# Kernel optimization log

Hardware: AMD Instinct MI355X
Metric: run time of the kernel (lower is better)

The kernel has to match this reference:

```python
import jax, jax.numpy as jnp
import numpy as np

# static sizes (see shape_source)
OBJ_N, WALL_N, FLOOR_N = 192, 16, 1
T = OBJ_N + WALL_N + FLOOR_N          # 209 total nodes
R = T * T - T                          # 43472 directed edges (no self loops)
D = 512
STEPS = 4                              # feat_update_step (1 group)
OBJ_IN, WALL_IN, FLOOR_IN, REL_IN = 42, 15, 16, 2

# buildMap: all-pairs meshgrid edges, self-loops removed, one-hot subj/obj maps
_nd = ~np.eye(T, dtype=bool)
_si, _oi = np.meshgrid(np.arange(T), np.arange(T), indexing='ij')
_subj_idx = _si[_nd]
_obj_idx = _oi[_nd]
SUBJ_MAP = jnp.asarray((np.arange(T)[:, None] == _subj_idx[None, :]).astype(np.float32))  # [T,R]
OBJ_MAP = jnp.asarray((np.arange(T)[:, None] == _obj_idx[None, :]).astype(np.float32))    # [T,R]
TOTAL_MAP = jnp.ones((T, T), jnp.float32)
REL_IDX = jnp.asarray(np.nonzero(_nd.reshape(-1))[0])  # [R] static gather indices


def setup_inputs():
    key = jax.random.key(0)
    ks = iter(jax.random.split(key, 64))
    def w(shape):
        return jax.random.normal(next(ks), shape, jnp.float32) * 0.01  # normal_(0, 0.01)
    inp = {
        'cat_object_feature': jax.random.normal(next(ks), (1, OBJ_N, OBJ_IN), jnp.float32),
        'cat_wall_feature': jax.random.normal(next(ks), (1, WALL_N, WALL_IN), jnp.float32),
        'cat_floor_feature': jax.random.normal(next(ks), (1, FLOOR_N, FLOOR_IN), jnp.float32),
        'cat_relation_feature': jax.random.normal(next(ks), (1, OBJ_N * OBJ_N, REL_IN), jnp.float32),
    }
    for name, din in [('obj', OBJ_IN), ('wall', WALL_IN), ('floor', FLOOR_IN), ('rel', REL_IN)]:
        inp[name + '_w1'] = w((din, D)); inp[name + '_b1'] = jnp.zeros((D,), jnp.float32)
        inp[name + '_w2'] = w((D, D));   inp[name + '_b2'] = jnp.zeros((D,), jnp.float32)
    inp['collect_w'] = w((5, D, D))                       # 5 _Collection_Unit fc weights
    inp['collect_b'] = jnp.zeros((5, D), jnp.float32)
    for name in ['tr', 'eu', 'sc']:
        inp[name + '_w1'] = w((D, D // 2)); inp[name + '_b1'] = jnp.zeros((D // 2,), jnp.float32)
        inp[name + '_w2'] = w((D // 2, 3)); inp[name + '_b2'] = jnp.zeros((3,), jnp.float32)
    return inp


def _mlp(x, w1, b1, w2, b2):
    return jax.nn.relu(x @ w1 + b1) @ w2 + b2


def _head(x, w1, b1, w2, b2):
    # Linear -> LeakyReLU(0.2) -> Dropout(eval: identity) -> Linear
    return jax.nn.leaky_relu(x @ w1 + b1, 0.2) @ w2 + b2


def _collect(src, attn, w, b):
    # _Collection_Unit: attn @ relu(fc(src)) / (row_sum + 1e-7)
    fc = jax.nn.relu(src @ w + b)
    return (attn @ fc) / (attn.sum(1, keepdims=True) + 1e-7)


def reference(cat_object_feature, cat_wall_feature, cat_floor_feature, cat_relation_feature,
              obj_w1, obj_b1, obj_w2, obj_b2, wall_w1, wall_b1, wall_w2, wall_b2,
              floor_w1, floor_b1, floor_w2, floor_b2, rel_w1, rel_b1, rel_w2, rel_b2,
              collect_w, collect_b, tr_w1, tr_b1, tr_w2, tr_b2,
              eu_w1, eu_b1, eu_w2, eu_b2, sc_w1, sc_b1, sc_w2, sc_b2):
    tot = jnp.concatenate([
        _mlp(cat_object_feature[0], obj_w1, obj_b1, obj_w2, obj_b2),
        _mlp(cat_wall_feature[0], wall_w1, wall_b1, wall_w2, wall_b2),
        _mlp(cat_floor_feature[0], floor_w1, floor_b1, floor_w2, floor_b2)], axis=0)  # [T,D]
    emb_rel = _mlp(cat_relation_feature[0], rel_w1, rel_b1, rel_w2, rel_b2)
    padded = jnp.pad(emb_rel.reshape(OBJ_N, OBJ_N, D),
                     ((0, T - OBJ_N), (0, T - OBJ_N), (0, 0)), constant_values=0.001)
    rel = padded.reshape(T * T, D)[REL_IDX]  # mask_total_relation_feature [R,D]

    for _ in range(STEPS):
        s_obj = _collect(tot, TOTAL_MAP, collect_w[4], collect_b[4])
        s_rs = _collect(rel, SUBJ_MAP, collect_w[0], collect_b[0])
        s_ro = _collect(rel, OBJ_MAP, collect_w[1], collect_b[1])
        new_tot = tot + (s_obj + s_rs + s_ro) / 3.0          # _Update_Unit: target + source
        s_os = _collect(tot, SUBJ_MAP.T, collect_w[2], collect_b[2])
        s_oo = _collect(tot, OBJ_MAP.T, collect_w[3], collect_b[3])
        rel = rel + (s_os + s_oo) / 2.0
        tot = new_tot

    obj = tot[:OBJ_N]  # object_mask select
    return jnp.concatenate([
        _head(obj, tr_w1, tr_b1, tr_w2, tr_b2),
        _head(obj, eu_w1, eu_b1, eu_w2, eu_b2),
        _head(obj, sc_w1, sc_b1, sc_w2, sc_b2)], axis=-1)  # [OBJ_N, 9]
```

## Files before the change

### kernel.cpp

```cpp
#include <hip/hip_runtime.h>
#include <stdint.h>

typedef unsigned short u16;
typedef __attribute__((ext_vector_type(4))) float f32x4;
typedef __attribute__((ext_vector_type(8))) short s16x8;
typedef __attribute__((ext_vector_type(4))) short s16x4;

#define DD (512*512)

__device__ inline u16 f2bf(float f) {
  uint32_t u = __float_as_uint(f);
  u = (u + 0x7FFFu + ((u >> 16) & 1u)) >> 16;
  return (u16)u;
}
__device__ inline float bflo(uint32_t w) { return __uint_as_float(w << 16); }
__device__ inline float bfhi(uint32_t w) { return __uint_as_float(w & 0xFFFF0000u); }
__device__ inline f32x4 relu4(f32x4 v) {
  f32x4 r;
  r.x = fmaxf(v.x, 0.f); r.y = fmaxf(v.y, 0.f);
  r.z = fmaxf(v.z, 0.f); r.w = fmaxf(v.w, 0.f);
  return r;
}
__device__ inline f32x4 bf4(const u16* p) {
  uint2 w = *(const uint2*)p;
  f32x4 r; r.x = bflo(w.x); r.y = bfhi(w.x); r.z = bflo(w.y); r.w = bfhi(w.y);
  return r;
}
__device__ inline s16x4 pack4(f32x4 v) {
  s16x4 o;
  o[0] = (short)f2bf(v.x); o[1] = (short)f2bf(v.y);
  o[2] = (short)f2bf(v.z); o[3] = (short)f2bf(v.w);
  return o;
}
__device__ inline void gload16(const void* g, void* l) {
  __builtin_amdgcn_global_load_lds(
      (const __attribute__((address_space(1))) void*)g,
      (__attribute__((address_space(3))) void*)l, 16, 0, 0);
}

struct PrepP {
  const float *xo, *xw, *xf;
  const float *ow1, *ob1, *ww1, *wb1, *fw1, *fb1;
  float* hid;
  const float* rw2; u16* rw2b;
  const float* cw; u16* cwT;
  const float* cb; const float* rb2;
  float *b0b, *b0p, *b1b, *b1p;
  const float *xr, *rw1, *rb1; u16* Hh;
};

__global__ __launch_bounds__(256) void kprep(PrepP pp) {
  __shared__ __align__(16) float plds[1088];
  const int bid = blockIdx.x;
  const int t = threadIdx.x;
  if (bid < 209) {
    int tc = bid;
    const float* x; const float* w; const float* b; int K;
    if (tc < 192)      { x = pp.xo + tc * 42;         w = pp.ow1; b = pp.ob1; K = 42; }
    else if (tc < 208) { x = pp.xw + (tc - 192) * 15; w = pp.ww1; b = pp.wb1; K = 15; }
    else               { x = pp.xf;                   w = pp.fw1; b = pp.fb1; K = 16; }
    float* xs = plds;
    if (t < K) xs[t] = x[t];
    __syncthreads();
    #pragma unroll
    for (int dd = 0; dd < 2; dd++) {
      int d = t + dd * 256;
      float acc = b[d];
      for (int k = 0; k < K; k++) acc = fmaf(xs[k], w[k * 512 + d], acc);
      pp.hid[(size_t)tc * 512 + d] = fmaxf(acc, 0.f);
    }
  } else if (bid < 337) {
    int g = (bid - 209) * 256 + t;
    f32x4 a = *(const f32x4*)&pp.rw2[(size_t)g * 8];
    f32x4 b = *(const f32x4*)&pp.rw2[(size_t)g * 8 + 4];
    s16x8 o;
    o[0] = (short)f2bf(a.x); o[1] = (short)f2bf(a.y); o[2] = (short)f2bf(a.z); o[3] = (short)f2bf(a.w);
    o[4] = (short)f2bf(b.x); o[5] = (short)f2bf(b.y); o[6] = (short)f2bf(b.z); o[7] = (short)f2bf(b.w);
    *(s16x8*)&pp.rw2b[(size_t)g * 8] = o;
  } else if (bid < 1617) {
    int local = bid - 337;
    int bx = local & 15, by = (local >> 4) & 15, bz = local >> 8;
    float (*tile)[33] = (float(*)[33])plds;
    const float* src = pp.cw + (size_t)bz * DD;
    int k0 = bx * 32, n0 = by * 32;
    #pragma unroll
    for (int i = 0; i < 4; i++) {
      int idx = t + i * 256; int r = idx >> 5, c = idx & 31;
      tile[r][c] = src[(size_t)(k0 + r) * 512 + n0 + c];
    }
    __syncthreads();
    #pragma unroll
    for (int i = 0; i < 4; i++) {
      int idx = t + i * 256; int r = idx >> 5, c = idx & 31;
      pp.cwT[((size_t)bz * 512 + n0 + r) * 512 + k0 + c] = f2bf(tile[c][r]);
    }
  } else if (bid < 1625) {
    int bx = bid - 1617;
    int dl = t & 63;
    int d = bx * 64 + dl;
    int kg = t >> 6;
    const float* W0 = pp.cw;
    const float* W1 = pp.cw + DD;
    float a0 = 0, p0 = 0, a1 = 0, p1 = 0;
    for (int k = kg * 128; k < (kg + 1) * 128; ++k) {
      float w0 = W0[(size_t)k * 512 + d], w1 = W1[(size_t)k * 512 + d], r = pp.rb2[k];
      a0 = fmaf(r, w0, a0); p0 += w0;
      a1 = fmaf(r, w1, a1); p1 += w1;
    }
    float (*red)[4][64] = (float(*)[4][64])plds;
    red[0][kg][dl] = a0; red[1][kg][dl] = p0; red[2][kg][dl] = a1; red[3][kg][dl] = p1;
    __syncthreads();
    if (kg == 0) {
      float s0  = red[0][0][dl] + red[0][1][dl] + red[0][2][dl] + red[0][3][dl];
      float sp0 = red[1][0][dl] + red[1][1][dl] + red[1][2][dl] + red[1][3][dl];
      float s1  = red[2][0][dl] + red[2][1][dl] + red[2][2][dl] + red[2][3][dl];
      float sp1 = red[3][0][dl] + red[3][1][dl] + red[3][2][dl] + red[3][3][dl];
      float bb0 = pp.cb[0 * 512 + d], bb1 = pp.cb[1 * 512 + d];
      pp.b0b[d] = s0 + bb0;
      pp.b0p[d] = 0.001f * sp0 + bb0;
      pp.b1b[d] = s1 + bb1;
      pp.b1p[d] = 0.001f * sp1 + bb1;
    }
  } else {
    int gid = (bid - 1625) * 256 + t;
    int m = gid >> 6;
    int dg = (gid & 63) * 8;
    float x0 = pp.xr[m * 2], x1 = pp.xr[m * 2 + 1];
    s16x8 o;
    #pragma unroll
    for (int j = 0; j < 8; j++) {
      int dd = dg + j;
      float v = fmaf(x0, pp.rw1[dd], fmaf(x1, pp.rw1[512 + dd], pp.rb1[dd]));
      o[j] = (short)f2bf(fmaxf(v, 0.f));
    }
    *(s16x8*)&pp.Hh[(size_t)m * 512 + dg] = o;
  }
}

struct SJob { const float* A; const float* B; const float* bias; float* C; u16* Cb; int M; int act; };
struct SJobs { SJob j[4]; int cum[5]; int njobs; };
struct PMJob { const u16* A; const u16* BT; u16* W; };
struct MidP { SJobs sj; PMJob mj[2]; };

__global__ __launch_bounds__(256) void kmid(MidP mp) {
  __shared__ __align__(16) u16 mlds[24576];
  const int t = threadIdx.x;
  if (blockIdx.x < 64) {
    int bi = blockIdx.x;
    int ji = 0;
    while (ji + 1 < mp.sj.njobs && bi >= mp.sj.cum[ji + 1]) ji++;
    SJob job = mp.sj.j[ji];
    int local = bi - mp.sj.cum[ji];
    int mt = local >> 3, nt = local & 7;
    int m0 = mt * 32, n0 = nt * 64;
    float* As = (float*)mlds;
    float* Bs = As + 32 * 36;
    int row = t >> 3;
    int cg  = (t & 7) * 8;
    f32x4 accA = {0.f,0.f,0.f,0.f}, accB = {0.f,0.f,0.f,0.f};
    for (int k0 = 0; k0 < 512; k0 += 32) {
      __syncthreads();
      {
        int ar = t >> 3, ac = (t & 7) * 4;
        f32x4 av = {0.f,0.f,0.f,0.f};
        if (m0 + ar < job.M) av = *(const f32x4*)&job.A[(size_t)(m0 + ar) * 512 + k0 + ac];
        *(f32x4*)&As[ar * 36 + ac] = av;
      }
      #pragma unroll
      for (int i = 0; i < 2; i++) {
        int idx = t + i * 256;
        int bk = idx >> 4, bn = (idx & 15) * 4;
        *(f32x4*)&Bs[bk * 64 + bn] = *(const f32x4*)&job.B[(size_t)(k0 + bk) * 512 + n0 + bn];
      }
      __syncthreads();
      #pragma unroll
      for (int kk = 0; kk < 32; kk += 4) {
        f32x4 a4 = *(const f32x4*)&As[row * 36 + kk];
        #pragma unroll
        for (int q = 0; q < 4; q++) {
          f32x4 b0 = *(const f32x4*)&Bs[(kk + q) * 64 + cg];
          f32x4 b1 = *(const f32x4*)&Bs[(kk + q) * 64 + cg + 4];
          float av = a4[q];
          accA += av * b0;
          accB += av * b1;
        }
      }
    }
    int r = m0 + row;
    if (r < job.M) {
      f32x4 b0 = {0.f,0.f,0.f,0.f}, b1 = {0.f,0.f,0.f,0.f};
      if (job.bias) { b0 = *(const f32x4*)&job.bias[n0 + cg]; b1 = *(const f32x4*)&job.bias[n0 + cg + 4]; }
      f32x4 o0 = accA + b0, o1 = accB + b1;
      if (job.act) { o0 = relu4(o0); o1 = relu4(o1); }
      *(f32x4*)&job.C[(size_t)r * 512 + n0 + cg]     = o0;
      *(f32x4*)&job.C[(size_t)r * 512 + n0 + cg + 4] = o1;
      if (job.Cb) {
        s16x8 ob;
        ob[0] = (short)f2bf(o0.x); ob[1] = (short)f2bf(o0.y);
        ob[2] = (short)f2bf(o0.z); ob[3] = (short)f2bf(o0.w);
        ob[4] = (short)f2bf(o1.x); ob[5] = (short)f2bf(o1.y);
        ob[6] = (short)f2bf(o1.z); ob[7] = (short)f2bf(o1.w);
        *(s16x8*)&job.Cb[(size_t)r * 512 + n0 + cg] = ob;
      }
    }
  } else {
    int bi = blockIdx.x - 64;
    int ji = bi >> 5;
    int local = bi & 31;
    PMJob job = mp.mj[ji];
    int m0 = (local >> 2) * 64, n0 = (local & 3) * 128;
    u16* smem = mlds;
    const int lane = t & 63;
    const int wave = t >> 6;
    const int wm = wave >> 1, wn = wave & 1;
    const int r16 = lane & 15;
    const int kq = lane >> 4;
    f32x4 acc[2][4];
    #pragma unroll
    for (int i = 0; i < 2; i++)
      #pragma unroll
      for (int j = 0; j < 4; j++) acc[i][j] = (f32x4){0.f,0.f,0.f,0.f};
    const u16* gA[2]; int laofs[2];
    const u16* gB[4]; int lbofs[4];
    #pragma unroll
    for (int i = 0; i < 2; i++) {
      int seg = i * 256 + t;
      int row = seg >> 3, s = seg & 7;
      gA[i] = job.A + (size_t)(m0 + row) * 512 + ((s ^ (row & 7)) << 3);
      laofs[i] = (i * 256 + (t & 192)) << 3;
    }
    #pragma unroll
    for (int i = 0; i < 4; i++) {
      int seg = i * 256 + t;
      int row = seg >> 3, s = seg & 7;
      gB[i] = job.BT + (size_t)(n0 + row) * 512 + ((s ^ (row & 7)) << 3);
      lbofs[i] = 4096 + ((i * 256 + (t & 192)) << 3);
    }
    #pragma unroll
    for (int i = 0; i < 2; i++) gload16(gA[i], smem + laofs[i]);
    #pragma unroll
    for (int i = 0; i < 4; i++) gload16(gB[i], smem + lbofs[i]);
    __syncthreads();
    int buf = 0;
    for (int it = 0; it < 8; ++it) {
      if (it < 7) {
        int nb = (buf ^ 1) * 12288;
        int k0n = (it + 1) * 64;
        #pragma unroll
        for (int i = 0; i < 2; i++) gload16(gA[i] + k0n, smem + nb + laofs[i]);
        #pragma unroll
        for (int i = 0; i < 4; i++) gload16(gB[i] + k0n, smem + nb + lbofs[i]);
      }
      const u16* Ab = smem + buf * 12288;
      const u16* Bb = Ab + 4096;
      #pragma unroll
      for (int kh = 0; kh < 2; kh++) {
        s16x8 af[2], bfr[4];
        #pragma unroll
        for (int i = 0; i < 2; i++) {
          int r = wm * 32 + i * 16 + r16;
          af[i] = *(const s16x8*)&Ab[r * 64 + (((kq + kh * 4) ^ (r & 7)) << 3)];
        }
        #pragma unroll
        for (int j = 0; j < 4; j++) {
          int r = wn * 64 + j * 16 + r16;
          bfr[j] = *(const s16x8*)&Bb[r * 64 + (((kq + kh * 4) ^ (r & 7)) << 3)];
        }
        #pragma unroll
        for (int i = 0; i < 2; i++)
          #pragma unroll
          for (int j = 0; j < 4; j++)
            acc[i][j] = __builtin_amdgcn_mfma_f32_16x16x32_bf16(af[i], bfr[j], acc[i][j], 0, 0, 0);
      }
      __syncthreads();
      buf ^= 1;
    }
    #pragma unroll
    for (int i = 0; i < 2; i++) {
      int rbase = m0 + wm * 32 + i * 16 + kq * 4;
      #pragma unroll
      for (int j = 0; j < 4; j++) {
        int col = n0 + wn * 64 + j * 16 + r16;
        s16x4 o;
        #pragma unroll
        for (int r = 0; r < 4; r++) o[r] = (short)f2bf(acc[i][j][r]);
        *(s16x4*)&job.W[(size_t)col * 512 + rbase] = o;
      }
    }
  }
}

__global__ __launch_bounds__(256) void kbig(const u16* __restrict__ Hh, const u16* __restrict__ WcT,
                                            u16* __restrict__ Q0, u16* __restrict__ Q1T) {
  __shared__ u16 smem[2 * 16384];
  const int bid = blockIdx.x;
  const int xcd = bid & 7;
  const int lp = bid >> 3;
  const int m0 = (xcd * 36 + (lp >> 3)) * 128;
  const int n0 = (lp & 7) * 128;
  const int t = threadIdx.x;
  const int lane = t & 63;
  const int wave = t >> 6;
  const int wm = wave >> 1, wn = wave & 1;
  const int r16 = lane & 15;
  const int kq = lane >> 4;
  f32x4 acc[4][4];
  #pragma unroll
  for (int i = 0; i < 4; i++)
    #pragma unroll
    for (int j = 0; j < 4; j++) acc[i][j] = (f32x4){0.f, 0.f, 0.f, 0.f};

  const u16* gA[4]; const u16* gB[4];
  int lofs[4];
  #pragma unroll
  for (int i = 0; i < 4; i++) {
    int seg = i * 256 + t;
    int row = seg >> 3, s = seg & 7;
    int sw = (s ^ (row & 7)) << 3;
    gA[i] = Hh  + (size_t)(m0 + row) * 512 + sw;
    gB[i] = WcT + (size_t)(n0 + row) * 512 + sw;
    lofs[i] = (i * 256 + (t & 192)) << 3;
  }
  #pragma unroll
  for (int i = 0; i < 4; i++) {
    gload16(gA[i], smem + lofs[i]);
    gload16(gB[i], smem + 8192 + lofs[i]);
  }
  __syncthreads();
  int buf = 0;
  for (int it = 0; it < 8; ++it) {
    if (it < 7) {
      int nb = (buf ^ 1) * 16384;
      int k0n = (it + 1) * 64;
      #pragma unroll
      for (int i = 0; i < 4; i++) {
        gload16(gA[i] + k0n, smem + nb + lofs[i]);
        gload16(gB[i] + k0n, smem + nb + 8192 + lofs[i]);
      }
    }
    const u16* Ab = smem + buf * 16384;
    const u16* Bb = Ab + 8192;
    #pragma unroll
    for (int kh = 0; kh < 2; kh++) {
      s16x8 af[4], bfr[4];
      #pragma unroll
      for (int i = 0; i < 4; i++) {
        int r = wm * 64 + i * 16 + r16;
        af[i] = *(const s16x8*)&Ab[r * 64 + (((kq + kh * 4) ^ (r & 7)) << 3)];
      }
      #pragma unroll
      for (int j = 0; j < 4; j++) {
        int r = wn * 64 + j * 16 + r16;
        bfr[j] = *(const s16x8*)&Bb[r * 64 + (((kq + kh * 4) ^ (r & 7)) << 3)];
      }
      #pragma unroll
      for (int i = 0; i < 4; i++)
        #pragma unroll
        for (int j = 0; j < 4; j++)
          acc[i][j] = __builtin_amdgcn_mfma_f32_16x16x32_bf16(af[i], bfr[j], acc[i][j], 0, 0, 0);
    }
    __syncthreads();
    buf ^= 1;
  }

  float* Cs = (float*)smem;
  const bool isQ1 = (n0 >= 512);
  #pragma unroll
  for (int c = 0; c < 4; c++) {
    __syncthreads();
    if ((c >> 1) == wm) {
      const int cbase = (c & 1) * 32;
      #pragma unroll
      for (int ii = 0; ii < 2; ii++) {
        const int i = (cbase >> 4) + ii;
        #pragma unroll
        for (int j = 0; j < 4; j++) {
          #pragma unroll
          for (int r = 0; r < 4; r++) {
            int rrow = i * 16 + (lane >> 4) * 4 + r - cbase;
            int ccol = wn * 64 + j * 16 + r16;
            Cs[rrow * 132 + ccol] = acc[i][j][r];
          }
        }
      }
    }
    __syncthreads();
    const int row = t >> 3, cg = (t & 7) * 16;
    const int gm = m0 + c * 32 + row;
    s16x8 o0, o1;
    #pragma unroll
    for (int x = 0; x < 8; x++) o0[x] = (short)f2bf(Cs[row * 132 + cg + x]);
    #pragma unroll
    for (int x = 0; x < 8; x++) o1[x] = (short)f2bf(Cs[row * 132 + cg + 8 + x]);
    u16* dst;
    if (!isQ1) {
      dst = Q0 + (size_t)gm * 512 + (n0 + cg);
    } else {
      int s = gm / 192, o = gm - s * 192;
      dst = Q1T + ((size_t)o * 192 + s) * 512 + (n0 - 512 + cg);
    }
    *(s16x8*)dst = o0;
    *(s16x8*)(dst + 8) = o1;
  }
}

struct MJob { const u16* A; const u16* BT; const float* bias; float* C; float* csum; int Mreal; int mode; };
struct MJobs { MJob j[8]; int cum[9]; int njobs; };

__global__ __launch_bounds__(256) void kmg(MJobs js) {
  int bi = blockIdx.x;
  int ji = 0;
  while (ji + 1 < js.njobs && bi >= js.cum[ji + 1]) ji++;
  MJob job = js.j[ji];
  int local = bi - js.cum[ji];
  int m0 = (local >> 3) * 64, n0 = (local & 7) * 64;

  __shared__ u16 smem[2 * 16384];
  const int t = threadIdx.x;
  const int lane = t & 63;
  const int wv = t >> 6;
  const int r16 = lane & 15;
  const int kq = lane >> 4;
  f32x4 acc[4];
  #pragma unroll
  for (int j = 0; j < 4; j++) acc[j] = (f32x4){0.f,0.f,0.f,0.f};

  const u16* gA[4]; const u16* gB[4]; int lofs[4];
  #pragma unroll
  for (int i = 0; i < 4; i++) {
    int seg = i * 256 + t;
    int row = seg >> 4, s = seg & 15;
    int sw = (s ^ (row & 15)) << 3;
    gA[i] = job.A  + (size_t)(m0 + row) * 512 + sw;
    gB[i] = job.BT + (size_t)(n0 + row) * 512 + sw;
    lofs[i] = (i * 256 + (t & 192)) << 3;
  }
  #pragma unroll
  for (int i = 0; i < 4; i++) {
    gload16(gA[i], smem + lofs[i]);
    gload16(gB[i], smem + 8192 + lofs[i]);
  }
  __syncthreads();
  int buf = 0;
  for (int it = 0; it < 4; ++it) {
    if (it < 3) {
      int nb = (buf ^ 1) * 16384;
      int k0n = (it + 1) * 128;
      #pragma unroll
      for (int i = 0; i < 4; i++) {
        gload16(gA[i] + k0n, smem + nb + lofs[i]);
        gload16(gB[i] + k0n, smem + nb + 8192 + lofs[i]);
      }
    }
    const u16* Ab = smem + buf * 16384;
    const u16* Bb = Ab + 8192;
    #pragma unroll
    for (int kh = 0; kh < 4; kh++) {
      int q = kh * 4 + kq;
      int ra = wv * 16 + r16;
      s16x8 af = *(const s16x8*)&Ab[ra * 128 + ((q ^ (ra & 15)) << 3)];
      #pragma unroll
      for (int j = 0; j < 4; j++) {
        int rb = j * 16 + r16;
        s16x8 bfr = *(const s16x8*)&Bb[rb * 128 + ((q ^ (rb & 15)) << 3)];
        acc[j] = __builtin_amdgcn_mfma_f32_16x16x32_bf16(af, bfr, acc[j], 0, 0, 0);
      }
    }
    __syncthreads();
    buf ^= 1;
  }

  float bj[4] = {0.f,0.f,0.f,0.f};
  if (job.mode) {
    #pragma unroll
    for (int j = 0; j < 4; j++) bj[j] = job.bias[n0 + j * 16 + r16];
  }
  if (job.mode == 2) {
    float fsum[4];
    #pragma unroll
    for (int j = 0; j < 4; j++) {
      fsum[j] = 0.f;
      #pragma unroll
      for (int r = 0; r < 4; r++) {
        int grow = m0 + wv * 16 + kq * 4 + r;
        if (grow < job.Mreal) fsum[j] += fmaxf(acc[j][r] + bj[j], 0.f);
      }
    }
    float (*red)[64] = (float(*)[64])smem;
    int cix = wv * 4 + kq;
    #pragma unroll
    for (int j = 0; j < 4; j++) red[cix][j * 16 + r16] = fsum[j];
    __syncthreads();
    if (t < 64) {
      float s = 0.f;
      #pragma unroll
      for (int c = 0; c < 16; c++) s += red[c][t];
      job.csum[(size_t)(m0 >> 6) * 512 + n0 + t] = s;
    }
    return;
  }
  #pragma unroll
  for (int j = 0; j < 4; j++) {
    int col = n0 + j * 16 + r16;
    #pragma unroll
    for (int r = 0; r < 4; r++) {
      int grow = m0 + wv * 16 + kq * 4 + r;
      if (grow < job.Mreal) {
        float v = acc[j][r] + bj[j];
        if (job.mode == 1) v = fmaxf(v, 0.f);
        job.C[(size_t)grow * 512 + col] = v;
      }
    }
  }
}

__global__ __launch_bounds__(128) void kpass(const u16* __restrict__ Q0, const u16* __restrict__ Q1T,
                                             const float* __restrict__ u0, const float* __restrict__ v0,
                                             const float* __restrict__ u1, const float* __restrict__ v1,
                                             const float* __restrict__ b0b, const float* __restrict__ b1b,
                                             const float* __restrict__ fc4part,
                                             float* __restrict__ part, float* __restrict__ sobj) {
  int z = blockIdx.z;
  int t = threadIdx.x;
  if (z == 2) {
    if (blockIdx.y != 0 || blockIdx.x >= 4) return;
    int d = blockIdx.x * 128 + t;
    sobj[d] = fc4part[d] + fc4part[512 + d] + fc4part[1024 + d] + fc4part[1536 + d];
    return;
  }
  int so = blockIdx.x;
  if (so >= 192) return;
  int chunk = blockIdx.y;
  int d = t * 4;
  const u16* Q = z ? Q1T : Q0;
  const float* fixtab  = z ? v1 : u0;
  const float* looptab = z ? u1 : v0;
  const float* bb = z ? b1b : b0b;
  f32x4 fix = *(const f32x4*)&fixtab[(size_t)so * 512 + d] + *(const f32x4*)&bb[d];
  f32x4 acc = {0.f,0.f,0.f,0.f};
  const u16* qbase = Q + ((size_t)so * 192 + chunk * 48) * 512 + d;
  const float* lbase = looptab + (size_t)(chunk * 48) * 512 + d;
  #pragma unroll 4
  for (int r = 0; r < 48; ++r) {
    f32x4 qa = bf4(qbase + (size_t)r * 512);
    f32x4 vv = *(const f32x4*)(lbase + (size_t)r * 512);
    f32x4 val = qa + fix + vv;
    acc.x += fmaxf(val.x, 0.f); acc.y += fmaxf(val.y, 0.f);
    acc.z += fmaxf(val.z, 0.f); acc.w += fmaxf(val.w, 0.f);
  }
  *(f32x4*)&part[(((size_t)z * 209 + so) * 4 + chunk) * 512 + d] = acc;
}

__global__ __launch_bounds__(128) void kfinish(const u16* __restrict__ Q0, const u16* __restrict__ Q1T,
                                               const float* __restrict__ u0, const float* __restrict__ v0,
                                               const float* __restrict__ u1, const float* __restrict__ v1,
                                               const float* __restrict__ b0b, const float* __restrict__ b0p,
                                               const float* __restrict__ b1b, const float* __restrict__ b1p,
                                               const float* __restrict__ part, const float* __restrict__ sobj,
                                               const float* __restrict__ fcS, const float* __restrict__ fcO,
                                               float* __restrict__ tot, float* __restrict__ addS,
                                               float* __restrict__ addO,
                                               u16* __restrict__ totb, u16* __restrict__ aSb,
                                               u16* __restrict__ aOb) {
  int tt = blockIdx.x;
  int t = threadIdx.x;
  int d = t * 4;
  size_t rowoff = (size_t)tt * 512 + d;
  f32x4 u0r = *(const f32x4*)&u0[rowoff];
  f32x4 v0r = *(const f32x4*)&v0[rowoff];
  f32x4 u1r = *(const f32x4*)&u1[rowoff];
  f32x4 v1r = *(const f32x4*)&v1[rowoff];
  f32x4 B0B = *(const f32x4*)&b0b[d];
  f32x4 B0P = *(const f32x4*)&b0p[d];
  f32x4 B1B = *(const f32x4*)&b1b[d];
  f32x4 B1P = *(const f32x4*)&b1p[d];
  f32x4 srs = {0.f,0.f,0.f,0.f}, sro = {0.f,0.f,0.f,0.f};
  if (tt < 192) {
    #pragma unroll
    for (int c = 0; c < 4; c++) {
      srs += *(const f32x4*)&part[(((size_t)0 * 209 + tt) * 4 + c) * 512 + d];
      sro += *(const f32x4*)&part[(((size_t)1 * 209 + tt) * 4 + c) * 512 + d];
    }
    for (int o = 192; o < 209; o++) srs += relu4(B0P + u0r + *(const f32x4*)&v0[(size_t)o * 512 + d]);
    for (int s = 192; s < 209; s++) sro += relu4(B1P + *(const f32x4*)&u1[(size_t)s * 512 + d] + v1r);
    f32x4 qd0 = bf4(Q0 + ((size_t)tt * 193) * 512 + d);
    srs -= relu4(qd0 + u0r + v0r + B0B);
    f32x4 qd1 = bf4(Q1T + ((size_t)tt * 193) * 512 + d);
    sro -= relu4(qd1 + u1r + v1r + B1B);
  } else {
    for (int o = 0; o < 209; o++) srs += relu4(B0P + u0r + *(const f32x4*)&v0[(size_t)o * 512 + d]);
    srs -= relu4(B0P + u0r + v0r);
    for (int s = 0; s < 209; s++) sro += relu4(B1P + *(const f32x4*)&u1[(size_t)s * 512 + d] + v1r);
    sro -= relu4(B1P + u1r + v1r);
  }
  const float inv209 = 1.0f / (float)(209.0 + 1e-7);
  const float inv208 = 1.0f / (float)(208.0 + 1e-7);
  const float invrel = 0.5f / (float)(1.0 + 1e-7);
  f32x4 so4 = *(const f32x4*)&sobj[d] * inv209;
  srs *= inv208;
  sro *= inv208;
  f32x4 tt4 = *(const f32x4*)&tot[rowoff];
  tt4 += (so4 + srs + sro) * (1.0f / 3.0f);
  *(f32x4*)&tot[rowoff] = tt4;
  f32x4 aS = *(const f32x4*)&addS[rowoff] + *(const f32x4*)&fcS[rowoff] * invrel;
  f32x4 aO = *(const f32x4*)&addO[rowoff] + *(const f32x4*)&fcO[rowoff] * invrel;
  *(f32x4*)&addS[rowoff] = aS;
  *(f32x4*)&addO[rowoff] = aO;
  *(s16x4*)&totb[rowoff] = pack4(tt4);
  *(s16x4*)&aSb[rowoff]  = pack4(aS);
  *(s16x4*)&aOb[rowoff]  = pack4(aO);
}

__global__ __launch_bounds__(256) void kheads(const float* __restrict__ tot,
    const float* __restrict__ w1a, const float* __restrict__ b1a, const float* __restrict__ w2a, const float* __restrict__ b2a,
    const float* __restrict__ w1b, const float* __restrict__ b1bb, const float* __restrict__ w2b, const float* __restrict__ b2b,
    const float* __restrict__ w1c, const float* __restrict__ b1c, const float* __restrict__ w2c, const float* __restrict__ b2c,
    float* __restrict__ out) {
  int row = blockIdx.x;
  int t = threadIdx.x;
  __shared__ float xs[512];
  xs[t] = tot[(size_t)row * 512 + t];
  xs[t + 256] = tot[(size_t)row * 512 + 256 + t];
  __syncthreads();
  const float* W1[3] = {w1a, w1b, w1c};
  const float* B1[3] = {b1a, b1bb, b1c};
  const float* W2[3] = {w2a, w2b, w2c};
  float p[9];
  #pragma unroll
  for (int hd = 0; hd < 3; hd++) {
    float a = B1[hd][t];
    for (int k = 0; k < 512; k += 4) {
      f32x4 x4 = *(const f32x4*)&xs[k];
      a = fmaf(x4.x, W1[hd][(size_t)(k + 0) * 256 + t], a);
      a = fmaf(x4.y, W1[hd][(size_t)(k + 1) * 256 + t], a);
      a = fmaf(x4.z, W1[hd][(size_t)(k + 2) * 256 + t], a);
      a = fmaf(x4.w, W1[hd][(size_t)(k + 3) * 256 + t], a);
    }
    float h = a > 0.f ? a : 0.2f * a;
    p[hd * 3 + 0] = h * W2[hd][t * 3 + 0];
    p[hd * 3 + 1] = h * W2[hd][t * 3 + 1];
    p[hd * 3 + 2] = h * W2[hd][t * 3 + 2];
  }
  __shared__ float red[9][256];
  #pragma unroll
  for (int c = 0; c < 9; c++) red[c][t] = p[c];
  __syncthreads();
  for (int s = 128; s > 0; s >>= 1) {
    if (t < s) {
      #pragma unroll
      for (int c = 0; c < 9; c++) red[c][t] += red[c][t + s];
    }
    __syncthreads();
  }
  if (t < 9) {
    const float* B2[3] = {b2a, b2b, b2c};
    out[(size_t)row * 9 + t] = red[t][0] + B2[t / 3][t % 3];
  }
}

extern "C" void kernel_launch(void* const* d_in, const int* in_sizes, int n_in,
                              void* d_out, int out_size, void* d_ws, size_t ws_size,
                              hipStream_t stream) {
  const float* xo  = (const float*)d_in[0];
  const float* xw  = (const float*)d_in[1];
  const float* xf  = (const float*)d_in[2];
  const float* xr  = (const float*)d_in[3];
  const float* ow1 = (const float*)d_in[4];
  const float* ob1 = (const float*)d_in[5];
  const float* ow2 = (const float*)d_in[6];
  const float* ob2 = (const float*)d_in[7];
  const float* ww1 = (const float*)d_in[8];
  const float* wb1 = (const float*)d_in[9];
  const float* ww2 = (const float*)d_in[10];
  const float* wb2 = (const float*)d_in[11];
  const float* fw1 = (const float*)d_in[12];
  const float* fb1 = (const float*)d_in[13];
  const float* fw2 = (const float*)d_in[14];
  const float* fb2 = (const float*)d_in[15];
  const float* rw1 = (const float*)d_in[16];
  const float* rb1 = (const float*)d_in[17];
  const float* rw2 = (const float*)d_in[18];
  const float* rb2 = (const float*)d_in[19];
  const float* cw  = (const float*)d_in[20];
  const float* cb  = (const float*)d_in[21];
  const float* tw1 = (const float*)d_in[22];
  const float* tb1 = (const float*)d_in[23];
  const float* tw2 = (const float*)d_in[24];
  const float* tb2 = (const float*)d_in[25];
  const float* ew1 = (const float*)d_in[26];
  const float* eb1 = (const float*)d_in[27];
  const float* ew2 = (const float*)d_in[28];
  const float* eb2 = (const float*)d_in[29];
  const float* sw1 = (const float*)d_in[30];
  const float* sb1 = (const float*)d_in[31];
  const float* sw2 = (const float*)d_in[32];
  const float* sb2 = (const float*)d_in[33];
  float* out = (float*)d_out;

  char* p = (char*)d_ws;
  auto alloc = [&](size_t bytes) { char* r = p; p += (bytes + 255) & ~(size_t)255; return r; };
  const size_t SZ = 209 * 512 * sizeof(float);
  const size_t BSZ = 256 * 512 * sizeof(u16);
  float* tot  = (float*)alloc(SZ);
  float* addS = (float*)alloc(SZ);
  float* addO = (float*)alloc(SZ);
  u16*   totb = (u16*)alloc(BSZ);
  u16*   aSb  = (u16*)alloc(BSZ);
  u16*   aOb  = (u16*)alloc(BSZ);
  float* fc4part = (float*)alloc(4 * 512 * sizeof(float));
  float* fcS  = (float*)alloc(SZ);
  float* fcO  = (float*)alloc(SZ);
  float* u0   = (float*)alloc(SZ);
  float* v0   = (float*)alloc(SZ);
  float* u1   = (float*)alloc(SZ);
  float* v1   = (float*)alloc(SZ);
  float* hid  = (float*)alloc(SZ);
  float* sobj = (float*)alloc(512 * sizeof(float));
  float* part = (float*)alloc((size_t)2 * 209 * 4 * 512 * sizeof(float));
  float* b0b  = (float*)alloc(512 * sizeof(float));
  float* b0p  = (float*)alloc(512 * sizeof(float));
  float* b1b  = (float*)alloc(512 * sizeof(float));
  float* b1p  = (float*)alloc(512 * sizeof(float));
  u16* rw2b = (u16*)alloc((size_t)DD * sizeof(u16));
  u16* cwT  = (u16*)alloc((size_t)5 * DD * sizeof(u16));
  u16* Hh  = (u16*)alloc((size_t)36864 * 512 * sizeof(u16));
  u16* WcT = (u16*)alloc((size_t)1024 * 512 * sizeof(u16));
  u16* Q0  = (u16*)alloc((size_t)36864 * 512 * sizeof(u16));
  u16* Q1T = (u16*)alloc((size_t)36864 * 512 * sizeof(u16));

  hipMemsetAsync(addS, 0, 2 * SZ + 3 * BSZ, stream);

  PrepP pp;
  pp.xo = xo; pp.xw = xw; pp.xf = xf;
  pp.ow1 = ow1; pp.ob1 = ob1; pp.ww1 = ww1; pp.wb1 = wb1; pp.fw1 = fw1; pp.fb1 = fb1;
  pp.hid = hid;
  pp.rw2 = rw2; pp.rw2b = rw2b;
  pp.cw = cw; pp.cwT = cwT;
  pp.cb = cb; pp.rb2 = rb2;
  pp.b0b = b0b; pp.b0p = b0p; pp.b1b = b1b; pp.b1p = b1p;
  pp.xr = xr; pp.rw1 = rw1; pp.rb1 = rb1; pp.Hh = Hh;
  kprep<<<10841, 256, 0, stream>>>(pp);

  MidP mp{};
  mp.sj.j[0] = { hid,             ow2, ob2, tot,             totb,             192, 0 };
  mp.sj.j[1] = { hid + 192 * 512, ww2, wb2, tot + 192 * 512, totb + 192 * 512,  16, 0 };
  mp.sj.j[2] = { hid + 208 * 512, fw2, fb2, tot + 208 * 512, totb + 208 * 512,   1, 0 };
  mp.sj.njobs = 3;
  mp.sj.cum[0] = 0;
  for (int i = 0; i < 3; i++) mp.sj.cum[i + 1] = mp.sj.cum[i] + ((mp.sj.j[i].M + 31) / 32) * 8;
  mp.mj[0] = { rw2b, cwT,      WcT };
  mp.mj[1] = { rw2b, cwT + DD, WcT + DD };
  kmid<<<128, 256, 0, stream>>>(mp);

  kbig<<<2304, 256, 0, stream>>>(Hh, WcT, Q0, Q1T);

  MJobs st{};
  st.j[0] = { totb, cwT + 4 * DD, cb + 4 * 512, nullptr, fc4part, 209, 2 };
  st.j[1] = { totb, cwT + 2 * DD, cb + 2 * 512, fcS, nullptr, 209, 1 };
  st.j[2] = { totb, cwT + 3 * DD, cb + 3 * 512, fcO, nullptr, 209, 1 };
  st.j[3] = { aSb,  cwT,          nullptr,      u0,  nullptr, 209, 0 };
  st.j[4] = { aOb,  cwT,          nullptr,      v0,  nullptr, 209, 0 };
  st.j[5] = { aSb,  cwT + DD,     nullptr,      u1,  nullptr, 209, 0 };
  st.j[6] = { aOb,  cwT + DD,     nullptr,      v1,  nullptr, 209, 0 };
  st.njobs = 7;
  st.cum[0] = 0;
  for (int i = 0; i < 7; i++) st.cum[i + 1] = st.cum[i] + 4 * 8;

  for (int step = 0; step < 4; step++) {
    kmg<<<st.cum[7], 256, 0, stream>>>(st);
    kpass<<<dim3(209, 4, 3), 128, 0, stream>>>(Q0, Q1T, u0, v0, u1, v1, b0b, b1b, fc4part, part, sobj);
    kfinish<<<209, 128, 0, stream>>>(Q0, Q1T, u0, v0, u1, v1, b0b, b0p, b1b, b1p,
                                     part, sobj, fcS, fcO, tot, addS, addO, totb, aSb, aOb);
  }

  kheads<<<192, 256, 0, stream>>>(tot, tw1, tb1, tw2, tb2, ew1, eb1, ew2, eb2, sw1, sb1, sw2, sb2, out);
}
```

Baseline: 399.4 us.

## Skip zero-input GEMMs in first step, single-buffer kbig, parallelize head MLPs

In step 0 the aS/aO accumulators are known zero, so u0/v0/u1/v1 are zeroed by an enlarged memset and kmg runs only the three tot-based jobs. kbig drops LDS double buffering for a single buffer with two barriers per K tile, which halves shared memory and may allow higher occupancy but no longer overlaps loads with compute. The head MLPs are recomputed with 768-thread blocks, one thread per head output, reading a transposed W1 prepared in kprep with vectorized row reads. The buffer layout is reordered so the memset covers u0..v1.

```diff
diff --git a/kernel.cpp b/kernel.cpp
--- a/kernel.cpp
+++ b/kernel.cpp
@@ -47,6 +47,7 @@
   const float* cb; const float* rb2;
   float *b0b, *b0p, *b1b, *b1p;
   const float *xr, *rw1, *rb1; u16* Hh;
+  const float *tw1, *ew1, *sw1; float* hW1T;
 };
 
 __global__ __launch_bounds__(256) void kprep(PrepP pp) {
@@ -121,7 +122,7 @@
       pp.b1b[d] = s1 + bb1;
       pp.b1p[d] = 0.001f * sp1 + bb1;
     }
-  } else {
+  } else if (bid < 10841) {
     int gid = (bid - 1625) * 256 + t;
     int m = gid >> 6;
     int dg = (gid & 63) * 8;
@@ -134,6 +135,24 @@
       o[j] = (short)f2bf(fmaxf(v, 0.f));
     }
     *(s16x8*)&pp.Hh[(size_t)m * 512 + dg] = o;
+  } else {
+    int local = bid - 10841;
+    int hd = local >> 7;
+    int tile_i = local & 127;
+    int k0 = (tile_i & 15) * 32, c0 = (tile_i >> 4) * 32;
+    const float* src = (hd == 0) ? pp.tw1 : (hd == 1) ? pp.ew1 : pp.sw1;
+    float (*tile)[33] = (float(*)[33])plds;
+    #pragma unroll
+    for (int i = 0; i < 4; i++) {
+      int idx = t + i * 256; int r = idx >> 5, c = idx & 31;
+      tile[r][c] = src[(size_t)(k0 + r) * 256 + c0 + c];
+    }
+    __syncthreads();
+    #pragma unroll
+    for (int i = 0; i < 4; i++) {
+      int idx = t + i * 256; int r = idx >> 5, c = idx & 31;
+      pp.hW1T[((size_t)hd * 256 + c0 + r) * 512 + k0 + c] = tile[c][r];
+    }
   }
 }
 
@@ -292,7 +311,7 @@
 
 __global__ __launch_bounds__(256) void kbig(const u16* __restrict__ Hh, const u16* __restrict__ WcT,
                                             u16* __restrict__ Q0, u16* __restrict__ Q1T) {
-  __shared__ u16 smem[2 * 16384];
+  __shared__ u16 smem[16384];
   const int bid = blockIdx.x;
   const int xcd = bid & 7;
   const int lp = bid >> 3;
@@ -321,25 +340,17 @@
     gB[i] = WcT + (size_t)(n0 + row) * 512 + sw;
     lofs[i] = (i * 256 + (t & 192)) << 3;
   }
-  #pragma unroll
-  for (int i = 0; i < 4; i++) {
-    gload16(gA[i], smem + lofs[i]);
-    gload16(gB[i], smem + 8192 + lofs[i]);
-  }
-  __syncthreads();
-  int buf = 0;
-  for (int it = 0; it < 8; ++it) {
-    if (it < 7) {
-      int nb = (buf ^ 1) * 16384;
-      int k0n = (it + 1) * 64;
-      #pragma unroll
-      for (int i = 0; i < 4; i++) {
-        gload16(gA[i] + k0n, smem + nb + lofs[i]);
-        gload16(gB[i] + k0n, smem + nb + 8192 + lofs[i]);
-      }
-    }
-    const u16* Ab = smem + buf * 16384;
-    const u16* Bb = Ab + 8192;
+
+  for (int k0 = 0; k0 < 512; k0 += 64) {
+    __syncthreads();
+    #pragma unroll
+    for (int i = 0; i < 4; i++) {
+      gload16(gA[i] + k0, smem + lofs[i]);
+      gload16(gB[i] + k0, smem + 8192 + lofs[i]);
+    }
+    __syncthreads();
+    const u16* Ab = smem;
+    const u16* Bb = smem + 8192;
     #pragma unroll
     for (int kh = 0; kh < 2; kh++) {
       s16x8 af[4], bfr[4];
@@ -359,8 +370,6 @@
         for (int j = 0; j < 4; j++)
           acc[i][j] = __builtin_amdgcn_mfma_f32_16x16x32_bf16(af[i], bfr[j], acc[i][j], 0, 0, 0);
     }
-    __syncthreads();
-    buf ^= 1;
   }
 
   float* Cs = (float*)smem;
@@ -611,50 +620,49 @@
   *(s16x4*)&aOb[rowoff]  = pack4(aO);
 }
 
-__global__ __launch_bounds__(256) void kheads(const float* __restrict__ tot,
-    const float* __restrict__ w1a, const float* __restrict__ b1a, const float* __restrict__ w2a, const float* __restrict__ b2a,
-    const float* __restrict__ w1b, const float* __restrict__ b1bb, const float* __restrict__ w2b, const float* __restrict__ b2b,
-    const float* __restrict__ w1c, const float* __restrict__ b1c, const float* __restrict__ w2c, const float* __restrict__ b2c,
+__global__ __launch_bounds__(768) void kheads2(const float* __restrict__ tot,
+    const float* __restrict__ hW1T,
+    const float* __restrict__ tb1, const float* __restrict__ eb1, const float* __restrict__ sb1,
+    const float* __restrict__ tw2, const float* __restrict__ ew2, const float* __restrict__ sw2,
+    const float* __restrict__ tb2, const float* __restrict__ eb2, const float* __restrict__ sb2,
     float* __restrict__ out) {
   int row = blockIdx.x;
   int t = threadIdx.x;
+  int hd = t >> 8, c = t & 255;
   __shared__ float xs[512];
-  xs[t] = tot[(size_t)row * 512 + t];
-  xs[t + 256] = tot[(size_t)row * 512 + 256 + t];
+  __shared__ float red[9][256];
+  if (t < 512) xs[t] = tot[(size_t)row * 512 + t];
   __syncthreads();
-  const float* W1[3] = {w1a, w1b, w1c};
-  const float* B1[3] = {b1a, b1bb, b1c};
-  const float* W2[3] = {w2a, w2b, w2c};
-  float p[9];
-  #pragma unroll
-  for (int hd = 0; hd < 3; hd++) {
-    float a = B1[hd][t];
-    for (int k = 0; k < 512; k += 4) {
-      f32x4 x4 = *(const f32x4*)&xs[k];
-      a = fmaf(x4.x, W1[hd][(size_t)(k + 0) * 256 + t], a);
-      a = fmaf(x4.y, W1[hd][(size_t)(k + 1) * 256 + t], a);
-      a = fmaf(x4.z, W1[hd][(size_t)(k + 2) * 256 + t], a);
-      a = fmaf(x4.w, W1[hd][(size_t)(k + 3) * 256 + t], a);
-    }
-    float h = a > 0.f ? a : 0.2f * a;
-    p[hd * 3 + 0] = h * W2[hd][t * 3 + 0];
-    p[hd * 3 + 1] = h * W2[hd][t * 3 + 1];
-    p[hd * 3 + 2] = h * W2[hd][t * 3 + 2];
-  }
-  __shared__ float red[9][256];
-  #pragma unroll
-  for (int c = 0; c < 9; c++) red[c][t] = p[c];
+  const float* B1 = (hd == 0) ? tb1 : (hd == 1) ? eb1 : sb1;
+  const float* W2 = (hd == 0) ? tw2 : (hd == 1) ? ew2 : sw2;
+  const float* w = hW1T + ((size_t)hd * 256 + c) * 512;
+  f32x4 a0 = {0.f,0.f,0.f,0.f}, a1 = {0.f,0.f,0.f,0.f};
+  for (int k = 0; k < 512; k += 8) {
+    f32x4 wa = *(const f32x4*)&w[k];
+    f32x4 wb = *(const f32x4*)&w[k + 4];
+    f32x4 xa = *(const f32x4*)&xs[k];
+    f32x4 xb = *(const f32x4*)&xs[k + 4];
+    a0 += wa * xa;
+    a1 += wb * xb;
+  }
+  f32x4 a4 = a0 + a1;
+  float a = a4.x + a4.y + a4.z + a4.w + B1[c];
+  float h = a > 0.f ? a : 0.2f * a;
+  red[hd * 3 + 0][c] = h * W2[c * 3 + 0];
+  red[hd * 3 + 1][c] = h * W2[c * 3 + 1];
+  red[hd * 3 + 2][c] = h * W2[c * 3 + 2];
   __syncthreads();
   for (int s = 128; s > 0; s >>= 1) {
-    if (t < s) {
-      #pragma unroll
-      for (int c = 0; c < 9; c++) red[c][t] += red[c][t + s];
-    }
-    __syncthreads();
-  }
-  if (t < 9) {
-    const float* B2[3] = {b2a, b2b, b2c};
-    out[(size_t)row * 9 + t] = red[t][0] + B2[t / 3][t % 3];
+    if (c < s) {
+      red[hd * 3 + 0][c] += red[hd * 3 + 0][c + s];
+      red[hd * 3 + 1][c] += red[hd * 3 + 1][c + s];
+      red[hd * 3 + 2][c] += red[hd * 3 + 2][c + s];
+    }
+    __syncthreads();
+  }
+  if (c < 3) {
+    const float* B2 = (hd == 0) ? tb2 : (hd == 1) ? eb2 : sb2;
+    out[(size_t)row * 9 + hd * 3 + c] = red[hd * 3 + c][0] + B2[c];
   }
 }
 
@@ -707,13 +715,13 @@
   u16*   totb = (u16*)alloc(BSZ);
   u16*   aSb  = (u16*)alloc(BSZ);
   u16*   aOb  = (u16*)alloc(BSZ);
-  float* fc4part = (float*)alloc(4 * 512 * sizeof(float));
-  float* fcS  = (float*)alloc(SZ);
-  float* fcO  = (float*)alloc(SZ);
   float* u0   = (float*)alloc(SZ);
   float* v0   = (float*)alloc(SZ);
   float* u1   = (float*)alloc(SZ);
   float* v1   = (float*)alloc(SZ);
+  float* fc4part = (float*)alloc(4 * 512 * sizeof(float));
+  float* fcS  = (float*)alloc(SZ);
+  float* fcO  = (float*)alloc(SZ);
   float* hid  = (float*)alloc(SZ);
   float* sobj = (float*)alloc(512 * sizeof(float));
   float* part = (float*)alloc((size_t)2 * 209 * 4 * 512 * sizeof(float));
@@ -721,6 +729,7 @@
   float* b0p  = (float*)alloc(512 * sizeof(float));
   float* b1b  = (float*)alloc(512 * sizeof(float));
   float* b1p  = (float*)alloc(512 * sizeof(float));
+  float* hW1T = (float*)alloc((size_t)3 * 256 * 512 * sizeof(float));
   u16* rw2b = (u16*)alloc((size_t)DD * sizeof(u16));
   u16* cwT  = (u16*)alloc((size_t)5 * DD * sizeof(u16));
   u16* Hh  = (u16*)alloc((size_t)36864 * 512 * sizeof(u16));
@@ -728,7 +737,7 @@
   u16* Q0  = (u16*)alloc((size_t)36864 * 512 * sizeof(u16));
   u16* Q1T = (u16*)alloc((size_t)36864 * 512 * sizeof(u16));
 
-  hipMemsetAsync(addS, 0, 2 * SZ + 3 * BSZ, stream);
+  hipMemsetAsync(addS, 0, 6 * SZ + 3 * BSZ, stream);
 
   PrepP pp;
   pp.xo = xo; pp.xw = xw; pp.xf = xf;
@@ -739,7 +748,8 @@
   pp.cb = cb; pp.rb2 = rb2;
   pp.b0b = b0b; pp.b0p = b0p; pp.b1b = b1b; pp.b1p = b1p;
   pp.xr = xr; pp.rw1 = rw1; pp.rb1 = rb1; pp.Hh = Hh;
-  kprep<<<10841, 256, 0, stream>>>(pp);
+  pp.tw1 = tw1; pp.ew1 = ew1; pp.sw1 = sw1; pp.hW1T = hW1T;
+  kprep<<<11225, 256, 0, stream>>>(pp);
 
   MidP mp{};
   mp.sj.j[0] = { hid,             ow2, ob2, tot,             totb,             192, 0 };
@@ -766,12 +776,16 @@
   st.cum[0] = 0;
   for (int i = 0; i < 7; i++) st.cum[i + 1] = st.cum[i] + 4 * 8;
 
+  MJobs st0 = st;
+  st0.njobs = 3;
+
   for (int step = 0; step < 4; step++) {
-    kmg<<<st.cum[7], 256, 0, stream>>>(st);
+    if (step == 0) kmg<<<st0.cum[3], 256, 0, stream>>>(st0);
+    else           kmg<<<st.cum[7], 256, 0, stream>>>(st);
     kpass<<<dim3(209, 4, 3), 128, 0, stream>>>(Q0, Q1T, u0, v0, u1, v1, b0b, b1b, fc4part, part, sobj);
     kfinish<<<209, 128, 0, stream>>>(Q0, Q1T, u0, v0, u1, v1, b0b, b0p, b1b, b1p,
                                      part, sobj, fcS, fcO, tot, addS, addO, totb, aSb, aOb);
   }
 
-  kheads<<<192, 256, 0, stream>>>(tot, tw1, tb1, tw2, tb2, ew1, eb1, ew2, eb2, sw1, sb1, sw2, sb2, out);
-}
+  kheads2<<<192, 768, 0, stream>>>(tot, hW1T, tb1, eb1, sb1, tw2, ew2, sw2, tb2, eb2, sb2, out);
+}
```

Result: slower. 427.5 us (+7.0%).
